# Optimization experiments

Hardware: AMD Instinct MI355X
Metric: run time of the kernel (lower is better)

Reference implementation:

```python
import jax, jax.numpy as jnp
import numpy as np

B = 1024        # number of graphs in batch
NNODES = 64     # nodes per graph
NODE = 4        # node feature size
EDGEF = 2       # edge feature size
HID = 32        # hidden_dim
NFACT = 3       # num_factories
NE = 1024       # edges per graph (self.edges list length)


def setup_inputs() -> dict:
    key = jax.random.key(0)
    ks = jax.random.split(key, 12)
    rng = np.random.default_rng(1)
    # per-graph edge list (self.edges in the torch module)
    edges = rng.integers(0, NNODES, size=(NE, 2))
    edges_src = jnp.asarray(edges[:, 0], dtype=jnp.int32)   # [NE]
    edges_dst = jnp.asarray(edges[:, 1], dtype=jnp.int32)   # [NE]
    # batched edge_index for EdgeConv: same per-graph edges offset by b*NNODES
    offs = np.arange(B, dtype=np.int64)[:, None] * NNODES   # [B,1]
    ei_src = (edges[:, 0][None, :] + offs).reshape(-1)
    ei_dst = (edges[:, 1][None, :] + offs).reshape(-1)
    edge_index = jnp.asarray(np.stack([ei_src, ei_dst], 0), dtype=jnp.int32)  # [2, B*NE]

    N = B * NNODES
    E = B * NE
    x = jax.random.normal(ks[0], (N, NODE), dtype=jnp.float32)
    edge_attr = jax.random.normal(ks[1], (E, EDGEF), dtype=jnp.float32)
    action = jax.random.uniform(ks[2], (B, NE + NFACT), dtype=jnp.float32)

    s = 0.1
    W1 = jax.random.normal(ks[3], (2 * NODE + EDGEF, HID), dtype=jnp.float32) * s
    b1 = jnp.zeros((HID,), jnp.float32)
    W2 = jax.random.normal(ks[4], (HID, HID), dtype=jnp.float32) * s
    b2 = jnp.zeros((HID,), jnp.float32)
    D = (NODE + HID) * 2 + 1  # 73
    Wl = jax.random.normal(ks[5], (D, HID), dtype=jnp.float32) * s
    bl = jnp.zeros((HID,), jnp.float32)
    Wv = jax.random.normal(ks[6], (HID, 1), dtype=jnp.float32) * s
    bv = jnp.zeros((1,), jnp.float32)

    return {"x": x, "edge_index": edge_index, "edge_attr": edge_attr,
            "action": action, "edges_src": edges_src, "edges_dst": edges_dst,
            "W1": W1, "b1": b1, "W2": W2, "b2": b2,
            "Wl": Wl, "bl": bl, "Wv": Wv, "bv": bv}


def reference(x, edge_index, edge_attr, action, edges_src, edges_dst,
              W1, b1, W2, b2, Wl, bl, Wv, bv):
    N = x.shape[0]
    src = edge_index[0]  # flow='target_to_source': x_i = x[src], aggregate at src
    dst = edge_index[1]
    # EdgeConv message: MLP(cat[x_i, x_j, edge_attr])
    tmp = jnp.concatenate([x[src], x[dst], edge_attr], axis=1)  # [E, 10]
    msg = jax.nn.relu(tmp @ W1 + b1) @ W2 + b2                  # [E, HID]
    x_pp = jax.ops.segment_sum(msg, src, num_segments=N)        # scatter-add
    # concat node feats with conv output, split into graphs
    h = jnp.concatenate([x, x_pp], axis=1).reshape(B, NNODES, NODE + HID)  # [B,NN,36]
    # gather per-edge endpoint features
    ef = jnp.concatenate([h[:, edges_src], h[:, edges_dst]], axis=2)       # [B,NE,72]
    # factory features: last NFACT nodes duplicated
    pf = jnp.concatenate([h[:, -NFACT:], h[:, -NFACT:]], axis=-1)          # [B,NF,72]
    feats = jnp.concatenate([ef, pf], axis=1)                               # [B,NE+NF,72]
    concat = jnp.concatenate([feats, action[..., None]], axis=-1)           # [B,NE+NF,73]
    hidden = jax.nn.relu(concat @ Wl + bl)                                  # [B,NE+NF,HID]
    v = hidden @ Wv + bv                                                    # [B,NE+NF,1]
    return jnp.sum(v, axis=1).squeeze(-1)                                   # [B]
```

## Files before the change

kernel.cpp:

```cpp
#include <hip/hip_runtime.h>

#define NNODES 64
#define HID 32
#define NFACT 3
#define NE 1024
#define NROWS (NE + NFACT)
#define TPB 256
#define STR 36
#define MAXTILES 128

#define WS_DEG  64
#define WS_TN   128
#define WS_PE   256

typedef short bf16x8 __attribute__((ext_vector_type(8)));
typedef float f32x4  __attribute__((ext_vector_type(4)));

__device__ __forceinline__ unsigned pack_bf2(float lo, float hi) {
    unsigned ul = __builtin_bit_cast(unsigned, lo);
    unsigned uh = __builtin_bit_cast(unsigned, hi);
    ul += 0x7fffu + ((ul >> 16) & 1u);
    uh += 0x7fffu + ((uh >> 16) & 1u);
    return (ul >> 16) | (uh & 0xffff0000u);
}
__device__ __forceinline__ short f2bf(float f) {
    unsigned u = __builtin_bit_cast(unsigned, f);
    u += 0x7fffu + ((u >> 16) & 1u);
    return (short)(u >> 16);
}
__device__ __forceinline__ float4 fma4(float a, float4 w, float4 c) {
    c.x = fmaf(a, w.x, c.x); c.y = fmaf(a, w.y, c.y);
    c.z = fmaf(a, w.z, c.z); c.w = fmaf(a, w.w, c.w);
    return c;
}

__global__ __launch_bounds__(TPB) void build_csr(const int* __restrict__ es,
                                                 const int* __restrict__ ed,
                                                 int* __restrict__ ws) {
    __shared__ int sdeg[NNODES], soff[NNODES], scnt[NNODES];
    const int tid = threadIdx.x;
    if (tid < NNODES) { sdeg[tid] = 0; scnt[tid] = 0; }
    if (tid < MAXTILES) ws[WS_TN + tid] = 0;
#pragma unroll 1
    for (int i = tid; i < MAXTILES * 16; i += TPB) ws[WS_PE + i] = 0xFFFF;
    __syncthreads();
#pragma unroll 1
    for (int e = tid; e < NE; e += TPB) atomicAdd(&sdeg[es[e]], 1);
    __syncthreads();
    if (tid == 0) {
        int run = 0;
#pragma unroll 1
        for (int n = 0; n < NNODES; n++) { soff[n] = run; run += (sdeg[n] + 15) >> 4; }
        ws[0] = run;
    }
    __syncthreads();
    if (tid < NNODES) {
        ws[WS_DEG + tid] = sdeg[tid];
        const int base = soff[tid], cnt = (sdeg[tid] + 15) >> 4;
#pragma unroll 1
        for (int j = 0; j < cnt; j++) ws[WS_TN + base + j] = tid;
    }
    __syncthreads();
#pragma unroll 1
    for (int e = tid; e < NE; e += TPB) {
        const int n = es[e];
        const int idx = atomicAdd(&scnt[n], 1);
        ws[WS_PE + soff[n] * 16 + idx] = e | (ed[e] << 16);
    }
}

__global__ __launch_bounds__(TPB, 4) void critic_fused(
    const float* __restrict__ x,
    const float* __restrict__ edge_attr,
    const float* __restrict__ action,
    const int*   __restrict__ es,
    const int*   __restrict__ ed,
    const float* __restrict__ W1,
    const float* __restrict__ b1,
    const float* __restrict__ W2,
    const float* __restrict__ b2,
    const float* __restrict__ Wl,
    const float* __restrict__ bl,
    const float* __restrict__ Wv,
    const float* __restrict__ bv,
    const int*   __restrict__ csr,
    float* __restrict__ out)
{
    const int b    = blockIdx.x;
    const int tid  = threadIdx.x;
    const int lane = tid & 63;
    const int wv   = tid >> 6;
    const int quad = lane >> 4;
    const int m16  = lane & 15;
    const int kh   = quad * 8;

    __shared__ float4 xs4[NNODES];
    __shared__ float  xpp[NNODES * STR];
    __shared__ float  qp0[NNODES * STR];
    __shared__ float  qp1[NNODES * STR];
    __shared__ float  W1s[10 * HID];
    __shared__ float  b1s[HID];
    __shared__ float  wred[TPB / 64];

    if (tid < NNODES) xs4[tid] = ((const float4*)x)[b * NNODES + tid];
    if (tid < 80) ((float4*)W1s)[tid] = ((const float4*)W1)[tid];
    if (tid < HID) b1s[tid] = b1[tid];
#pragma unroll 1
    for (int i = tid; i < NNODES * STR; i += TPB) xpp[i] = 0.0f;
    __syncthreads();

    const int n  = tid & 63;
    const int k0 = (tid >> 6) * 8;

    {
        const float4 xv = xs4[n];
        const float4* b1v = (const float4*)&b1s[k0];
        float4 q1a = b1v[0], q1b = b1v[1];
        float4 q2a = make_float4(0.f, 0.f, 0.f, 0.f), q2b = q2a;
#pragma unroll 1
        for (int i = 0; i < 4; i++) {
            const float xi = (i == 0) ? xv.x : (i == 1) ? xv.y : (i == 2) ? xv.z : xv.w;
            const float4* wa = (const float4*)&W1s[i * HID + k0];
            const float4* wb = (const float4*)&W1s[(4 + i) * HID + k0];
            q1a = fma4(xi, wa[0], q1a); q1b = fma4(xi, wa[1], q1b);
            q2a = fma4(xi, wb[0], q2a); q2b = fma4(xi, wb[1], q2b);
        }
        float4* q1w = (float4*)&qp0[n * STR + k0];
        float4* q2w = (float4*)&qp1[n * STR + k0];
        q1w[0] = q1a; q1w[1] = q1b;
        q2w[0] = q2a; q2w[1] = q2b;
    }

    bf16x8 bP1a, bP1b, bP2a, bP2b;
#pragma unroll
    for (int j = 0; j < 8; j++) {
        bP1a[j] = f2bf(Wl[(4 + kh + j) * HID + m16]);
        bP1b[j] = f2bf(Wl[(4 + kh + j) * HID + 16 + m16]);
        bP2a[j] = f2bf(Wl[(40 + kh + j) * HID + m16]);
        bP2b[j] = f2bf(Wl[(40 + kh + j) * HID + 16 + m16]);
    }
    float wx1a[4], wx1b[4], wx2a[4], wx2b[4];
#pragma unroll
    for (int i = 0; i < 4; i++) {
        wx1a[i] = Wl[i * HID + m16];
        wx1b[i] = Wl[i * HID + 16 + m16];
        wx2a[i] = Wl[(36 + i) * HID + m16];
        wx2b[i] = Wl[(36 + i) * HID + 16 + m16];
    }
    const float blca = bl[m16], blcb = bl[16 + m16];
    float b2k[8];
#pragma unroll
    for (int j = 0; j < 8; j++) b2k[j] = b2[kh + j];
    const int   mrow = wv * 16 + m16;
    const float dn   = (float)csr[WS_DEG + mrow];
    __syncthreads();

    {
        const float2* ea2 = (const float2*)edge_attr + (size_t)b * NE;
        const int NW = TPB / 64;

        const float4* w8p = (const float4*)&W1s[8 * HID + kh];
        const float4* w9p = (const float4*)&W1s[9 * HID + kh];
        const float4 w8a = w8p[0], w8b = w8p[1];
        const float4 w9a = w9p[0], w9b = w9p[1];

        bf16x8 bf0, bf1;
#pragma unroll
        for (int j = 0; j < 8; j++) {
            bf0[j] = f2bf(W2[(kh + j) * HID + m16]);
            bf1[j] = f2bf(W2[(kh + j) * HID + 16 + m16]);
        }

        const int  ntiles = csr[0];
        const int* tn  = csr + WS_TN;
        const int* pep = csr + WS_PE;

#pragma unroll 1
        for (int t = wv; t < ntiles; t += NW) {
            const int raw  = pep[t * 16 + m16];
            const int node = tn[t];
            const int e    = raw & 0xFFFF;
            const bool pad = (e == 0xFFFF);
            const int d0   = raw >> 16;
            const float2 ea = ea2[pad ? 0 : e];

            const float4* Ap = (const float4*)&qp0[node * STR + kh];
            const float4  A0 = Ap[0], A1 = Ap[1];
            const float4* Gp = (const float4*)&qp1[d0 * STR + kh];
            const float4  G0 = Gp[0], G1 = Gp[1];

            const float h0 = fmaxf(A0.x + G0.x + ea.x * w8a.x + ea.y * w9a.x, 0.f);
            const float h1 = fmaxf(A0.y + G0.y + ea.x * w8a.y + ea.y * w9a.y, 0.f);
            const float h2 = fmaxf(A0.z + G0.z + ea.x * w8a.z + ea.y * w9a.z, 0.f);
            const float h3 = fmaxf(A0.w + G0.w + ea.x * w8a.w + ea.y * w9a.w, 0.f);
            const float h4 = fmaxf(A1.x + G1.x + ea.x * w8b.x + ea.y * w9b.x, 0.f);
            const float h5 = fmaxf(A1.y + G1.y + ea.x * w8b.y + ea.y * w9b.y, 0.f);
            const float h6 = fmaxf(A1.z + G1.z + ea.x * w8b.z + ea.y * w9b.z, 0.f);
            const float h7 = fmaxf(A1.w + G1.w + ea.x * w8b.w + ea.y * w9b.w, 0.f);

            uint4 packed;
            packed.x = pad ? 0u : pack_bf2(h0, h1);
            packed.y = pad ? 0u : pack_bf2(h2, h3);
            packed.z = pad ? 0u : pack_bf2(h4, h5);
            packed.w = pad ? 0u : pack_bf2(h6, h7);
            const bf16x8 af = __builtin_bit_cast(bf16x8, packed);

            f32x4 c0 = {0.f, 0.f, 0.f, 0.f};
            f32x4 c1 = {0.f, 0.f, 0.f, 0.f};
            c0 = __builtin_amdgcn_mfma_f32_16x16x32_bf16(af, bf0, c0, 0, 0, 0);
            c1 = __builtin_amdgcn_mfma_f32_16x16x32_bf16(af, bf1, c1, 0, 0, 0);

            float s0 = c0[0] + c0[1] + c0[2] + c0[3];
            float s1 = c1[0] + c1[1] + c1[2] + c1[3];
            s0 += __shfl_xor(s0, 16); s0 += __shfl_xor(s0, 32);
            s1 += __shfl_xor(s1, 16); s1 += __shfl_xor(s1, 32);
            if (lane < 32)
                atomicAdd(&xpp[node * STR + lane], (lane < 16) ? s0 : s1);
        }
    }
    __syncthreads();

    {
        const float4* xr = (const float4*)&xpp[mrow * STR + kh];
        float4 x0 = xr[0], x1 = xr[1];
        x0.x = fmaf(dn, b2k[0], x0.x); x0.y = fmaf(dn, b2k[1], x0.y);
        x0.z = fmaf(dn, b2k[2], x0.z); x0.w = fmaf(dn, b2k[3], x0.w);
        x1.x = fmaf(dn, b2k[4], x1.x); x1.y = fmaf(dn, b2k[5], x1.y);
        x1.z = fmaf(dn, b2k[6], x1.z); x1.w = fmaf(dn, b2k[7], x1.w);
        uint4 packed;
        packed.x = pack_bf2(x0.x, x0.y);
        packed.y = pack_bf2(x0.z, x0.w);
        packed.z = pack_bf2(x1.x, x1.y);
        packed.w = pack_bf2(x1.z, x1.w);
        const bf16x8 af = __builtin_bit_cast(bf16x8, packed);

        f32x4 c1a, c1b, c2a, c2b;
#pragma unroll
        for (int r = 0; r < 4; r++) {
            const float4 xv = xs4[wv * 16 + quad * 4 + r];
            float a0 = blca, a1 = blcb, a2 = 0.f, a3 = 0.f;
#pragma unroll
            for (int i = 0; i < 4; i++) {
                const float xi = (i == 0) ? xv.x : (i == 1) ? xv.y : (i == 2) ? xv.z : xv.w;
                a0 = fmaf(xi, wx1a[i], a0);
                a1 = fmaf(xi, wx1b[i], a1);
                a2 = fmaf(xi, wx2a[i], a2);
                a3 = fmaf(xi, wx2b[i], a3);
            }
            c1a[r] = a0; c1b[r] = a1; c2a[r] = a2; c2b[r] = a3;
        }
        c1a = __builtin_amdgcn_mfma_f32_16x16x32_bf16(af, bP1a, c1a, 0, 0, 0);
        c1b = __builtin_amdgcn_mfma_f32_16x16x32_bf16(af, bP1b, c1b, 0, 0, 0);
        c2a = __builtin_amdgcn_mfma_f32_16x16x32_bf16(af, bP2a, c2a, 0, 0, 0);
        c2b = __builtin_amdgcn_mfma_f32_16x16x32_bf16(af, bP2b, c2b, 0, 0, 0);

#pragma unroll
        for (int r = 0; r < 4; r++) {
            const int row = wv * 16 + quad * 4 + r;
            qp0[row * STR + m16]      = c1a[r];
            qp0[row * STR + 16 + m16] = c1b[r];
            qp1[row * STR + m16]      = c2a[r];
            qp1[row * STR + 16 + m16] = c2b[r];
        }
    }
    __syncthreads();

    float vsum = 0.0f;
    {
        const float* actb = action + (size_t)b * NROWS;
        const float bvv = bv[0];
        const float* Wl72 = Wl + 72 * HID;
#pragma unroll 1
        for (int i = 0; i < 4; i++) {
            const int r = tid + i * TPB;
            const int na = es[r], nb = ed[r];
            const float a = actb[r];
            const float4* p1v = (const float4*)&qp0[na * STR];
            const float4* p2v = (const float4*)&qp1[nb * STR];
            float v0 = bvv, v1 = 0.0f;
#pragma unroll 1
            for (int q = 0; q < 8; q += 2) {
                const float4 pa0 = p1v[q],     pb0 = p2v[q];
                const float4 pa1 = p1v[q + 1], pb1 = p2v[q + 1];
                const int k = q * 4;
                v0 += fmaxf(pa0.x + pb0.x + a * Wl72[k+0], 0.f) * Wv[k+0];
                v1 += fmaxf(pa0.y + pb0.y + a * Wl72[k+1], 0.f) * Wv[k+1];
                v0 += fmaxf(pa0.z + pb0.z + a * Wl72[k+2], 0.f) * Wv[k+2];
                v1 += fmaxf(pa0.w + pb0.w + a * Wl72[k+3], 0.f) * Wv[k+3];
                v0 += fmaxf(pa1.x + pb1.x + a * Wl72[k+4], 0.f) * Wv[k+4];
                v1 += fmaxf(pa1.y + pb1.y + a * Wl72[k+5], 0.f) * Wv[k+5];
                v0 += fmaxf(pa1.z + pb1.z + a * Wl72[k+6], 0.f) * Wv[k+6];
                v1 += fmaxf(pa1.w + pb1.w + a * Wl72[k+7], 0.f) * Wv[k+7];
            }
            vsum += v0 + v1;
        }
        if (tid < NFACT) {
            const int r = NE + tid;
            const int na = NNODES - NFACT + tid;
            const float a = actb[r];
            const float4* p1v = (const float4*)&qp0[na * STR];
            const float4* p2v = (const float4*)&qp1[na * STR];
            float v = bvv;
#pragma unroll 1
            for (int q = 0; q < 8; q++) {
                const float4 pa = p1v[q], pb = p2v[q];
                const int k = q * 4;
                v += fmaxf(pa.x + pb.x + a * Wl72[k+0], 0.f) * Wv[k+0];
                v += fmaxf(pa.y + pb.y + a * Wl72[k+1], 0.f) * Wv[k+1];
                v += fmaxf(pa.z + pb.z + a * Wl72[k+2], 0.f) * Wv[k+2];
                v += fmaxf(pa.w + pb.w + a * Wl72[k+3], 0.f) * Wv[k+3];
            }
            vsum += v;
        }
    }

#pragma unroll
    for (int off = 32; off > 0; off >>= 1)
        vsum += __shfl_down(vsum, off, 64);
    if ((tid & 63) == 0) wred[tid >> 6] = vsum;
    __syncthreads();
    if (tid == 0) {
        float t = 0.0f;
#pragma unroll
        for (int w = 0; w < TPB / 64; w++) t += wred[w];
        out[b] = t;
    }
}

extern "C" void kernel_launch(void* const* d_in, const int* in_sizes, int n_in,
                              void* d_out, int out_size, void* d_ws, size_t ws_size,
                              hipStream_t stream) {
    const float* x         = (const float*)d_in[0];
    const float* edge_attr = (const float*)d_in[2];
    const float* action    = (const float*)d_in[3];
    const int*   es        = (const int*)d_in[4];
    const int*   ed        = (const int*)d_in[5];
    const float* W1        = (const float*)d_in[6];
    const float* b1        = (const float*)d_in[7];
    const float* W2        = (const float*)d_in[8];
    const float* b2        = (const float*)d_in[9];
    const float* Wl        = (const float*)d_in[10];
    const float* bl        = (const float*)d_in[11];
    const float* Wv        = (const float*)d_in[12];
    const float* bv        = (const float*)d_in[13];
    float* out = (float*)d_out;
    int*   ws  = (int*)d_ws;

    build_csr<<<dim3(1), dim3(TPB), 0, stream>>>(es, ed, ws);
    critic_fused<<<dim3(out_size), dim3(TPB), 0, stream>>>(
        x, edge_attr, action, es, ed, W1, b1, W2, b2, Wl, bl, Wv, bv, ws, out);
}
```

Before: 137.5 us.

## Process two 16-edge tiles per wave using 32x32x16 MFMA

The edge-message phase now handles two CSR tiles (32 edges) per wave iteration with 32x32x16 bf16 MFMAs, so all 64 lanes do useful work and no atomics are masked off. The CSR packing is reworked to 12-bit edge ids plus dst and src node ids, so each lane can find its own tile's node, and padding slots carry the node id. The offset scan in build_csr becomes a wave shuffle scan. The message loop also moves ahead of the Wl register loads, which may lower register pressure. The risk is more work per lane in the gather and ReLU step, and a 12-bit edge field that only holds while NE stays below 4096.

```diff
diff --git a/kernel.cpp b/kernel.cpp
--- a/kernel.cpp
+++ b/kernel.cpp
@@ -15,6 +15,7 @@
 
 typedef short bf16x8 __attribute__((ext_vector_type(8)));
 typedef float f32x4  __attribute__((ext_vector_type(4)));
+typedef float f32x16 __attribute__((ext_vector_type(16)));
 
 __device__ __forceinline__ unsigned pack_bf2(float lo, float hi) {
     unsigned ul = __builtin_bit_cast(unsigned, lo);
@@ -42,30 +43,40 @@
     if (tid < NNODES) { sdeg[tid] = 0; scnt[tid] = 0; }
     if (tid < MAXTILES) ws[WS_TN + tid] = 0;
 #pragma unroll 1
-    for (int i = tid; i < MAXTILES * 16; i += TPB) ws[WS_PE + i] = 0xFFFF;
+    for (int i = tid; i < MAXTILES * 16; i += TPB) ws[WS_PE + i] = 0xFFF;
     __syncthreads();
 #pragma unroll 1
     for (int e = tid; e < NE; e += TPB) atomicAdd(&sdeg[es[e]], 1);
     __syncthreads();
-    if (tid == 0) {
-        int run = 0;
-#pragma unroll 1
-        for (int n = 0; n < NNODES; n++) { soff[n] = run; run += (sdeg[n] + 15) >> 4; }
-        ws[0] = run;
-    }
-    __syncthreads();
     if (tid < NNODES) {
+        const int cnt = (sdeg[tid] + 15) >> 4;
+        int scan = cnt;
+#pragma unroll
+        for (int o = 1; o < 64; o <<= 1) {
+            const int v = __shfl_up(scan, o);
+            if (tid >= o) scan += v;
+        }
+        soff[tid] = scan - cnt;
         ws[WS_DEG + tid] = sdeg[tid];
+        if (tid == NNODES - 1) ws[0] = scan;
+    }
+    __syncthreads();
+    if (tid < NNODES) {
         const int base = soff[tid], cnt = (sdeg[tid] + 15) >> 4;
-#pragma unroll 1
-        for (int j = 0; j < cnt; j++) ws[WS_TN + base + j] = tid;
+        const int padv = 0xFFF | (tid << 18);
+#pragma unroll 1
+        for (int j = 0; j < cnt; j++) {
+            ws[WS_TN + base + j] = tid;
+#pragma unroll 1
+            for (int s = 0; s < 16; s++) ws[WS_PE + (base + j) * 16 + s] = padv;
+        }
     }
     __syncthreads();
 #pragma unroll 1
     for (int e = tid; e < NE; e += TPB) {
         const int n = es[e];
         const int idx = atomicAdd(&scnt[n], 1);
-        ws[WS_PE + soff[n] * 16 + idx] = e | (ed[e] << 16);
+        ws[WS_PE + soff[n] * 16 + idx] = e | (ed[e] << 12) | (n << 18);
     }
 }
 
@@ -130,6 +141,96 @@
         q1w[0] = q1a; q1w[1] = q1b;
         q2w[0] = q2a; q2w[1] = q2b;
     }
+    __syncthreads();
+
+    {
+        const float2* ea2 = (const float2*)edge_attr + (size_t)b * NE;
+        const int NW  = TPB / 64;
+        const int klo = (lane >> 5) * 8;
+        const int n32 = lane & 31;
+
+        const float4* w8l = (const float4*)&W1s[8 * HID + klo];
+        const float4* w8h = (const float4*)&W1s[8 * HID + 16 + klo];
+        const float4* w9l = (const float4*)&W1s[9 * HID + klo];
+        const float4* w9h = (const float4*)&W1s[9 * HID + 16 + klo];
+        const float4 w8a = w8l[0], w8b = w8l[1], w8c = w8h[0], w8d = w8h[1];
+        const float4 w9a = w9l[0], w9b = w9l[1], w9c = w9h[0], w9d = w9h[1];
+
+        bf16x8 bfA, bfB;
+#pragma unroll
+        for (int j = 0; j < 8; j++) {
+            bfA[j] = f2bf(W2[(klo + j) * HID + n32]);
+            bfB[j] = f2bf(W2[(16 + klo + j) * HID + n32]);
+        }
+
+        const int  ntiles = csr[0];
+        const int  np     = (ntiles + 1) >> 1;
+        const int* tn  = csr + WS_TN;
+        const int* pep = csr + WS_PE;
+
+#pragma unroll 1
+        for (int p = wv; p < np; p += NW) {
+            const int raw = pep[p * 32 + n32];
+            const int tA  = tn[2 * p];
+            const int tB  = tn[2 * p + 1];
+            const int e    = raw & 0xFFF;
+            const bool pad = (e == 0xFFF);
+            const int d0   = (raw >> 12) & 63;
+            const int nd   = (raw >> 18) & 63;
+            const float2 ea = ea2[pad ? 0 : e];
+
+            const float4* A1 = (const float4*)&qp0[nd * STR + klo];
+            const float4* A2 = (const float4*)&qp0[nd * STR + 16 + klo];
+            const float4* G1 = (const float4*)&qp1[d0 * STR + klo];
+            const float4* G2 = (const float4*)&qp1[d0 * STR + 16 + klo];
+            const float4 a0 = A1[0], a1 = A1[1], a2 = A2[0], a3 = A2[1];
+            const float4 g0 = G1[0], g1 = G1[1], g2 = G2[0], g3 = G2[1];
+
+            const float hx0 = fmaxf(a0.x + g0.x + ea.x * w8a.x + ea.y * w9a.x, 0.f);
+            const float hx1 = fmaxf(a0.y + g0.y + ea.x * w8a.y + ea.y * w9a.y, 0.f);
+            const float hx2 = fmaxf(a0.z + g0.z + ea.x * w8a.z + ea.y * w9a.z, 0.f);
+            const float hx3 = fmaxf(a0.w + g0.w + ea.x * w8a.w + ea.y * w9a.w, 0.f);
+            const float hx4 = fmaxf(a1.x + g1.x + ea.x * w8b.x + ea.y * w9b.x, 0.f);
+            const float hx5 = fmaxf(a1.y + g1.y + ea.x * w8b.y + ea.y * w9b.y, 0.f);
+            const float hx6 = fmaxf(a1.z + g1.z + ea.x * w8b.z + ea.y * w9b.z, 0.f);
+            const float hx7 = fmaxf(a1.w + g1.w + ea.x * w8b.w + ea.y * w9b.w, 0.f);
+            const float hy0 = fmaxf(a2.x + g2.x + ea.x * w8c.x + ea.y * w9c.x, 0.f);
+            const float hy1 = fmaxf(a2.y + g2.y + ea.x * w8c.y + ea.y * w9c.y, 0.f);
+            const float hy2 = fmaxf(a2.z + g2.z + ea.x * w8c.z + ea.y * w9c.z, 0.f);
+            const float hy3 = fmaxf(a2.w + g2.w + ea.x * w8c.w + ea.y * w9c.w, 0.f);
+            const float hy4 = fmaxf(a3.x + g3.x + ea.x * w8d.x + ea.y * w9d.x, 0.f);
+            const float hy5 = fmaxf(a3.y + g3.y + ea.x * w8d.y + ea.y * w9d.y, 0.f);
+            const float hy6 = fmaxf(a3.z + g3.z + ea.x * w8d.z + ea.y * w9d.z, 0.f);
+            const float hy7 = fmaxf(a3.w + g3.w + ea.x * w8d.w + ea.y * w9d.w, 0.f);
+
+            uint4 pkA, pkB;
+            pkA.x = pad ? 0u : pack_bf2(hx0, hx1);
+            pkA.y = pad ? 0u : pack_bf2(hx2, hx3);
+            pkA.z = pad ? 0u : pack_bf2(hx4, hx5);
+            pkA.w = pad ? 0u : pack_bf2(hx6, hx7);
+            pkB.x = pad ? 0u : pack_bf2(hy0, hy1);
+            pkB.y = pad ? 0u : pack_bf2(hy2, hy3);
+            pkB.z = pad ? 0u : pack_bf2(hy4, hy5);
+            pkB.w = pad ? 0u : pack_bf2(hy6, hy7);
+            const bf16x8 afA = __builtin_bit_cast(bf16x8, pkA);
+            const bf16x8 afB = __builtin_bit_cast(bf16x8, pkB);
+
+            f32x16 c;
+#pragma unroll
+            for (int j = 0; j < 16; j++) c[j] = 0.0f;
+            c = __builtin_amdgcn_mfma_f32_32x32x16_bf16(afA, bfA, c, 0, 0, 0);
+            c = __builtin_amdgcn_mfma_f32_32x32x16_bf16(afB, bfB, c, 0, 0, 0);
+
+            float sA = ((c[0] + c[1]) + (c[2] + c[3])) + ((c[4] + c[5]) + (c[6] + c[7]));
+            float sB = ((c[8] + c[9]) + (c[10] + c[11])) + ((c[12] + c[13]) + (c[14] + c[15]));
+            sA += __shfl_xor(sA, 32);
+            sB += __shfl_xor(sB, 32);
+            const int   nst = (lane < 32) ? tA : tB;
+            const float sv  = (lane < 32) ? sA : sB;
+            atomicAdd(&xpp[nst * STR + n32], sv);
+        }
+    }
+    __syncthreads();
 
     bf16x8 bP1a, bP1b, bP2a, bP2b;
 #pragma unroll
@@ -153,72 +254,6 @@
     for (int j = 0; j < 8; j++) b2k[j] = b2[kh + j];
     const int   mrow = wv * 16 + m16;
     const float dn   = (float)csr[WS_DEG + mrow];
-    __syncthreads();
-
-    {
-        const float2* ea2 = (const float2*)edge_attr + (size_t)b * NE;
-        const int NW = TPB / 64;
-
-        const float4* w8p = (const float4*)&W1s[8 * HID + kh];
-        const float4* w9p = (const float4*)&W1s[9 * HID + kh];
-        const float4 w8a = w8p[0], w8b = w8p[1];
-        const float4 w9a = w9p[0], w9b = w9p[1];
-
-        bf16x8 bf0, bf1;
-#pragma unroll
-        for (int j = 0; j < 8; j++) {
-            bf0[j] = f2bf(W2[(kh + j) * HID + m16]);
-            bf1[j] = f2bf(W2[(kh + j) * HID + 16 + m16]);
-        }
-
-        const int  ntiles = csr[0];
-        const int* tn  = csr + WS_TN;
-        const int* pep = csr + WS_PE;
-
-#pragma unroll 1
-        for (int t = wv; t < ntiles; t += NW) {
-            const int raw  = pep[t * 16 + m16];
-            const int node = tn[t];
-            const int e    = raw & 0xFFFF;
-            const bool pad = (e == 0xFFFF);
-            const int d0   = raw >> 16;
-            const float2 ea = ea2[pad ? 0 : e];
-
-            const float4* Ap = (const float4*)&qp0[node * STR + kh];
-            const float4  A0 = Ap[0], A1 = Ap[1];
-            const float4* Gp = (const float4*)&qp1[d0 * STR + kh];
-            const float4  G0 = Gp[0], G1 = Gp[1];
-
-            const float h0 = fmaxf(A0.x + G0.x + ea.x * w8a.x + ea.y * w9a.x, 0.f);
-            const float h1 = fmaxf(A0.y + G0.y + ea.x * w8a.y + ea.y * w9a.y, 0.f);
-            const float h2 = fmaxf(A0.z + G0.z + ea.x * w8a.z + ea.y * w9a.z, 0.f);
-            const float h3 = fmaxf(A0.w + G0.w + ea.x * w8a.w + ea.y * w9a.w, 0.f);
-            const float h4 = fmaxf(A1.x + G1.x + ea.x * w8b.x + ea.y * w9b.x, 0.f);
-            const float h5 = fmaxf(A1.y + G1.y + ea.x * w8b.y + ea.y * w9b.y, 0.f);
-            const float h6 = fmaxf(A1.z + G1.z + ea.x * w8b.z + ea.y * w9b.z, 0.f);
-            const float h7 = fmaxf(A1.w + G1.w + ea.x * w8b.w + ea.y * w9b.w, 0.f);
-
-            uint4 packed;
-            packed.x = pad ? 0u : pack_bf2(h0, h1);
-            packed.y = pad ? 0u : pack_bf2(h2, h3);
-            packed.z = pad ? 0u : pack_bf2(h4, h5);
-            packed.w = pad ? 0u : pack_bf2(h6, h7);
-            const bf16x8 af = __builtin_bit_cast(bf16x8, packed);
-
-            f32x4 c0 = {0.f, 0.f, 0.f, 0.f};
-            f32x4 c1 = {0.f, 0.f, 0.f, 0.f};
-            c0 = __builtin_amdgcn_mfma_f32_16x16x32_bf16(af, bf0, c0, 0, 0, 0);
-            c1 = __builtin_amdgcn_mfma_f32_16x16x32_bf16(af, bf1, c1, 0, 0, 0);
-
-            float s0 = c0[0] + c0[1] + c0[2] + c0[3];
-            float s1 = c1[0] + c1[1] + c1[2] + c1[3];
-            s0 += __shfl_xor(s0, 16); s0 += __shfl_xor(s0, 32);
-            s1 += __shfl_xor(s1, 16); s1 += __shfl_xor(s1, 32);
-            if (lane < 32)
-                atomicAdd(&xpp[node * STR + lane], (lane < 16) ? s0 : s1);
-        }
-    }
-    __syncthreads();
 
     {
         const float4* xr = (const float4*)&xpp[mrow * STR + kh];
```

After: 132.1 us. 3.9% less time.
